# Optimization experiments

Measured on AMD Instinct MI355X. Metric: run time of the kernel, lower is better.

The kernel has to match this reference:

```python
import jax, jax.numpy as jnp
import numpy as np

IDIM = 128
ODIM = 128
G = 8          # deformable groups
KH = KW = 3
K = KH * KW


def conv3x3(x, w, b):
    # x: [B,C,H,W], w: [O,I,3,3], stride 1, pad 1
    y = jax.lax.conv_general_dilated(x, w, (1, 1), ((1, 1), (1, 1)),
                                     dimension_numbers=('NCHW', 'OIHW', 'NCHW'))
    return y + b[None, :, None, None]


def deform_conv_v2(x, offset, mask, w, b):
    # x: [B,C,H,W]; offset: [B,2*G*K,H,W]; mask: [B,G*K,H,W] (pre-sigmoid)
    B, C, H, W = x.shape
    Cg = C // G
    off = offset.reshape(B, G, 2 * K, H, W)
    dy = off[:, :, 0::2]            # [B,G,K,H,W]
    dx = off[:, :, 1::2]
    m = jax.nn.sigmoid(mask).reshape(B, G, K, H, W)

    ky, kx = jnp.meshgrid(jnp.arange(KH), jnp.arange(KW), indexing='ij')
    ky = ky.reshape(K).astype(x.dtype)
    kx = kx.reshape(K).astype(x.dtype)
    hh = jnp.arange(H, dtype=x.dtype)
    ww = jnp.arange(W, dtype=x.dtype)
    # sampling positions (stride 1, pad 1, dilation 1)
    py = dy + (ky[:, None, None] + hh[None, :, None] - 1.0)   # [B,G,K,H,W]
    px = dx + (kx[:, None, None] + ww[None, None, :] - 1.0)

    y0 = jnp.floor(py)
    x0 = jnp.floor(px)
    ly = py - y0
    lx = px - x0

    x_flat = x.reshape(B, G, Cg, H * W)

    def gather(yi, xi):
        valid = ((yi >= 0) & (yi < H) & (xi >= 0) & (xi < W)).astype(x.dtype)
        yc = jnp.clip(yi, 0, H - 1).astype(jnp.int32)
        xc = jnp.clip(xi, 0, W - 1).astype(jnp.int32)
        idx = (yc * W + xc).reshape(B, G, 1, K * H * W)
        v = jnp.take_along_axis(x_flat, jnp.broadcast_to(idx, (B, G, Cg, K * H * W)), axis=3)
        return v.reshape(B, G, Cg, K, H, W) * valid[:, :, None]

    # bilinear interpolation with zero padding, fused with modulation mask
    v = (gather(y0, x0) * ((1 - ly) * (1 - lx))[:, :, None]
         + gather(y0, x0 + 1) * ((1 - ly) * lx)[:, :, None]
         + gather(y0 + 1, x0) * (ly * (1 - lx))[:, :, None]
         + gather(y0 + 1, x0 + 1) * (ly * lx)[:, :, None])
    v = v * m[:, :, None]                                      # [B,G,Cg,K,H,W]

    wr = w.reshape(w.shape[0], G, Cg, K)
    out = jnp.einsum('bgckhw,ogck->bohw', v, wr)
    return out + b[None, :, None, None]


def setup_inputs() -> dict:
    key = jax.random.key(0)
    ks = jax.random.split(key, 12)
    B, H, W = 2, 96, 96
    s = 0.05
    return {
        'R1': jax.random.normal(ks[0], (B, IDIM, H, W), jnp.float32),
        'Q0': jax.random.normal(ks[1], (B, IDIM, H, W), jnp.float32),
        'w1': jax.random.normal(ks[2], (ODIM, IDIM, 3, 3), jnp.float32) * s,
        'b1': jax.random.normal(ks[3], (ODIM,), jnp.float32) * s,
        'w2': jax.random.normal(ks[4], (ODIM, ODIM, 3, 3), jnp.float32) * s,
        'b2': jax.random.normal(ks[5], (ODIM,), jnp.float32) * s,
        'w_om': jax.random.normal(ks[6], (G * 3 * K, ODIM, 3, 3), jnp.float32) * s,
        'b_om': jax.random.normal(ks[7], (G * 3 * K,), jnp.float32) * s,
        'w_dcn': jax.random.normal(ks[8], (ODIM, IDIM, 3, 3), jnp.float32) * s,
        'b_dcn': jax.random.normal(ks[9], (ODIM,), jnp.float32) * s,
        'w_rq': jax.random.normal(ks[10], (ODIM, 2 * ODIM, 3, 3), jnp.float32) * s,
        'b_rq': jax.random.normal(ks[11], (ODIM,), jnp.float32) * s,
    }


def reference(R1, Q0, w1, b1, w2, b2, w_om, b_om, w_dcn, b_dcn, w_rq, b_rq):
    off = jax.nn.relu(conv3x3(R1 - Q0, w1, b1))
    off = jax.nn.relu(conv3x3(off, w2, b2))
    om = conv3x3(off, w_om, b_om)                 # [B, 3*G*K, H, W]
    o1, o2, mask = jnp.split(om, 3, axis=1)
    offset = jnp.concatenate([o1, o2], axis=1)    # [B, 2*G*K, H, W]
    fea = jax.nn.relu(deform_conv_v2(R1, offset, mask, w_dcn, b_dcn))
    fused = jnp.concatenate([fea, Q0], axis=1)
    return jax.nn.relu(conv3x3(fused, w_rq, b_rq))
```

## Files before the change

kernel.cpp:

```cpp
#include <hip/hip_runtime.h>

#define HH 96
#define WW 96
#define HW 9216
#define NPIX 18432
#define OMC 216
#define PP 9604

typedef __attribute__((ext_vector_type(8))) short short8x;
typedef __attribute__((ext_vector_type(8))) unsigned short ushort8x;
typedef __attribute__((ext_vector_type(4))) float f32x4;

__device__ __forceinline__ f32x4 mfma16(short8x a, short8x b, f32x4 c) {
    return __builtin_amdgcn_mfma_f32_16x16x32_bf16(a, b, c, 0, 0, 0);
}
__device__ __forceinline__ unsigned short f2bf(float f) {
    unsigned int u = __float_as_uint(f);
    u = (u + 0x7FFFu + ((u >> 16) & 1u)) >> 16;
    return (unsigned short)u;
}
__device__ __forceinline__ float bf2f(unsigned short b) {
    return __uint_as_float((unsigned int)b << 16);
}
__device__ __forceinline__ void split2(float v, unsigned short& h, unsigned short& l) {
    h = f2bf(v);
    l = f2bf(v - bf2f(h));
}
__device__ __forceinline__ void gld_lds16(const unsigned short* src, unsigned short* dst) {
    __builtin_amdgcn_global_load_lds(
        (const __attribute__((address_space(1))) unsigned int*)src,
        (__attribute__((address_space(3))) unsigned int*)dst, 16, 0, 0);
}

__global__ __launch_bounds__(256) void zero_borders(
    unsigned short* __restrict__ diffb,
    unsigned short* __restrict__ t1,
    unsigned short* __restrict__ catb)
{
    int i = blockIdx.x * 256 + threadIdx.x;
    if (i >= 776) return;
    int b = i / 388, r = i % 388;
    int y, x;
    if      (r < 98)  { y = 0;          x = r; }
    else if (r < 196) { y = 97;         x = r - 98; }
    else if (r < 292) { y = r - 196 + 1; x = 0; }
    else              { y = r - 292 + 1; x = 97; }
    size_t P = (size_t)b * PP + (size_t)y * 98 + x;
    ushort8x z = {};
    #pragma unroll
    for (int c = 0; c < 32; ++c) *(ushort8x*)&diffb[P * 256 + c * 8] = z;
    #pragma unroll
    for (int c = 0; c < 32; ++c) *(ushort8x*)&t1[P * 256 + c * 8] = z;
    #pragma unroll
    for (int c = 0; c < 64; ++c) *(ushort8x*)&catb[P * 512 + c * 8] = z;
}

__global__ __launch_bounds__(256) void prep_acts(
    const float* __restrict__ R1, const float* __restrict__ Q0,
    unsigned short* __restrict__ r1b,
    unsigned short* __restrict__ diffb,
    unsigned short* __restrict__ cat)
{
    __shared__ float tR[128][64];
    __shared__ float tQ[128][64];
    int tid = threadIdx.x;
    int p0  = blockIdx.x * 64;
    int b   = p0 / HW;
    int rem0 = p0 % HW;

    for (int e = tid; e < 2048; e += 256) {
        int c = e >> 4, j = e & 15;
        size_t base = ((size_t)(b * 128 + c)) * HW + rem0;
        *(float4*)&tR[c][j * 4] = *(const float4*)(R1 + base + j * 4);
        *(float4*)&tQ[c][j * 4] = *(const float4*)(Q0 + base + j * 4);
    }
    __syncthreads();

    int p = tid & 63, half = tid >> 6;
    int c0 = half * 32;
    int pix = p0 + p;
    int rm = pix % HW, yy = rm / 96, xx = rm % 96;
    size_t P = (size_t)b * PP + (size_t)(yy + 1) * 98 + xx + 1;
    ushort8x rb[4], dh[4], dl[4], qh[4], ql[4];
    #pragma unroll
    for (int cc = 0; cc < 32; ++cc) {
        float r = tR[c0 + cc][p], q = tQ[c0 + cc][p];
        rb[cc >> 3][cc & 7] = f2bf(r);
        unsigned short h, l;
        split2(r - q, h, l); dh[cc >> 3][cc & 7] = h; dl[cc >> 3][cc & 7] = l;
        split2(q, h, l);     qh[cc >> 3][cc & 7] = h; ql[cc >> 3][cc & 7] = l;
    }
    #pragma unroll
    for (int i = 0; i < 4; ++i) {
        *(ushort8x*)&r1b[(size_t)pix * 128 + c0 + i * 8] = rb[i];
        *(ushort8x*)&diffb[P * 256 +       c0 + i * 8] = dh[i];
        *(ushort8x*)&diffb[P * 256 + 128 + c0 + i * 8] = dl[i];
        *(ushort8x*)&cat [P * 512 + 128 + c0 + i * 8] = qh[i];
        *(ushort8x*)&cat [P * 512 + 384 + c0 + i * 8] = ql[i];
    }
}

__global__ __launch_bounds__(256) void prep_w(
    const float* __restrict__ w1, const float* __restrict__ w2,
    const float* __restrict__ wom, const float* __restrict__ bom,
    const float* __restrict__ wrq, const float* __restrict__ wdcn,
    unsigned short* __restrict__ p1, unsigned short* __restrict__ p2,
    unsigned short* __restrict__ pom, unsigned short* __restrict__ prq,
    unsigned short* __restrict__ pdcn, float* __restrict__ bomp)
{
    int idx = blockIdx.x * 256 + threadIdx.x;
    unsigned short h, l;
    if (idx < 147456) {
        int t = idx / 16384, o = (idx >> 7) & 127, ci = idx & 127;
        int src = (o * 128 + ci) * 9 + t;
        split2(w1[src], h, l);  p1[idx] = h;  p1[idx + 147456] = l;
        split2(w2[src], h, l);  p2[idx] = h;  p2[idx + 147456] = l;
        int dd = o * 1152 + ((ci >> 4) * 9 + t) * 16 + (ci & 15);
        split2(wdcn[src], h, l); pdcn[dd] = h; pdcn[dd + 147456] = l;
    }
    if (idx < 294912) {
        {
            int t = idx / 32768, o = (idx >> 7) & 255, ci = idx & 127;
            float v = (o < OMC) ? wom[(o * 128 + ci) * 9 + t] : 0.f;
            split2(v, h, l); pom[idx] = h; pom[idx + 294912] = l;
        }
        {
            int t = idx / 32768, o = (idx >> 8) & 127, ci = idx & 255;
            split2(wrq[(o * 256 + ci) * 9 + t], h, l);
            prq[idx] = h; prq[idx + 294912] = l;
        }
    }
    if (idx < 256) bomp[idx] = (idx < OMC) ? bom[idx] : 0.f;
}

template<int CIN, int COUTP, int MODE, bool RELU>
__global__ __launch_bounds__(256, 2) void conv_mfma(
    const unsigned short* __restrict__ in,
    const unsigned short* __restrict__ wpk,
    const float* __restrict__ bias,
    void* __restrict__ outv)
{
    constexpr int NKC = CIN / 32;
    constexpr int NSTEP = 9 * NKC;
    const size_t WPLANE = (size_t)9 * COUTP * CIN;

    __shared__ __align__(16) unsigned short s_buf[3][3072 + 8192];

    int tid = threadIdx.x;
    int wid = tid >> 6, lane = tid & 63;
    int r = lane & 15, q = lane >> 4;
    int bid = blockIdx.x;
    int swz = (bid & 7) * 48 + (bid >> 3);
    int rowid = swz >> 1, half = swz & 1;
    int b = rowid / 96, y = rowid % 96;
    int x0 = half * 48;
    int nbase = blockIdx.y * 128;

    auto stage = [&](int buf, int step) {
        int t = step / NKC, kc = step - t * NKC;
        int dy = t / 3 - 1, dx = t % 3 - 1;
        unsigned short* sb = &s_buf[buf][0];
        {
            int j = tid;
            int m = j >> 7, pl = (j >> 6) & 1, L = j & 63;
            int px = m * 16 + (L & 15), qd = L >> 4;
            const unsigned short* src = in +
                ((size_t)b * PP + (size_t)(y + 1 + dy) * 98 + (x0 + 1 + dx + px)) * (2 * CIN)
                + pl * CIN + kc * 32 + qd * 8;
            gld_lds16(src, sb + (size_t)(wid * 64) * 8);
        }
        if (tid < 128) {
            int j = 256 + tid;
            int m = j >> 7, pl = (j >> 6) & 1, L = j & 63;
            int px = m * 16 + (L & 15), qd = L >> 4;
            const unsigned short* src = in +
                ((size_t)b * PP + (size_t)(y + 1 + dy) * 98 + (x0 + 1 + dx + px)) * (2 * CIN)
                + pl * CIN + kc * 32 + qd * 8;
            gld_lds16(src, sb + (size_t)(256 + wid * 64) * 8);
        }
        const unsigned short* wbase = wpk + ((size_t)t * COUTP + nbase) * CIN + kc * 32;
        #pragma unroll
        for (int c = 0; c < 4; ++c) {
            int j = c * 256 + tid;
            int ni = (j >> 7) & 1, pl = (j >> 6) & 1, L = j & 63;
            int rr = L & 15, qq = L >> 4;
            const unsigned short* src = wbase + (size_t)pl * WPLANE
                + (size_t)(c * 32 + ni * 16 + rr) * CIN + qq * 8;
            gld_lds16(src, sb + 3072 + (size_t)(c * 256 + wid * 64) * 8);
        }
    };

    f32x4 acc[3][2] = {};

    auto compute = [&](int buf) {
        const unsigned short* sb = &s_buf[buf][0];
        short8x AH[3], AL[3], BH[2], BL[2];
        #pragma unroll
        for (int m = 0; m < 3; ++m) {
            AH[m] = *(const short8x*)(sb + m * 1024 + lane * 8);
            AL[m] = *(const short8x*)(sb + m * 1024 + 512 + lane * 8);
        }
        #pragma unroll
        for (int n = 0; n < 2; ++n) {
            BH[n] = *(const short8x*)(sb + 3072 + wid * 2048 + n * 1024 + lane * 8);
            BL[n] = *(const short8x*)(sb + 3072 + wid * 2048 + n * 1024 + 512 + lane * 8);
        }
        #pragma unroll
        for (int m = 0; m < 3; ++m) {
            #pragma unroll
            for (int n = 0; n < 2; ++n) {
                acc[m][n] = mfma16(AH[m], BH[n], acc[m][n]);
                acc[m][n] = mfma16(AL[m], BH[n], acc[m][n]);
                acc[m][n] = mfma16(AH[m], BL[n], acc[m][n]);
            }
        }
    };

    stage(0, 0);
    stage(1, 1);
    if (tid < 128) asm volatile("s_waitcnt vmcnt(6)" ::: "memory");
    else           asm volatile("s_waitcnt vmcnt(5)" ::: "memory");
    __builtin_amdgcn_s_barrier();

    for (int k = 0; k < NSTEP; ++k) {
        const int nb = k + 2;
        if (nb < NSTEP) stage(nb % 3, nb);
        compute(k % 3);
        if (k + 1 < NSTEP) {
            if (nb < NSTEP) {
                if (tid < 128) asm volatile("s_waitcnt vmcnt(6)" ::: "memory");
                else           asm volatile("s_waitcnt vmcnt(5)" ::: "memory");
            } else {
                asm volatile("s_waitcnt vmcnt(0)" ::: "memory");
            }
            __builtin_amdgcn_s_barrier();
        }
    }

    #pragma unroll
    for (int m = 0; m < 3; ++m) {
        #pragma unroll
        for (int n = 0; n < 2; ++n) {
            int o = nbase + wid * 32 + n * 16 + r;
            float bv = bias[o];
            #pragma unroll
            for (int j = 0; j < 4; ++j) {
                int px = m * 16 + q * 4 + j;
                int xx = x0 + px;
                float v = acc[m][n][j] + bv;
                if (RELU) v = fmaxf(v, 0.f);
                if (MODE == 0) {
                    size_t P = (size_t)b * PP + (size_t)(y + 1) * 98 + xx + 1;
                    unsigned short h, l; split2(v, h, l);
                    ((unsigned short*)outv)[P * 2 * COUTP + o] = h;
                    ((unsigned short*)outv)[P * 2 * COUTP + COUTP + o] = l;
                } else if (MODE == 1) {
                    if (o < OMC)
                        ((unsigned short*)outv)[((size_t)b * HW + y * 96 + xx) * OMC + o] = f2bf(v);
                } else {
                    ((float*)outv)[((size_t)b * 128 + o) * HW + y * 96 + xx] = v;
                }
            }
        }
    }
}

__global__ __launch_bounds__(256, 3) void deform_mfma(
    const unsigned short* __restrict__ xb,
    const unsigned short* __restrict__ omf,
    const unsigned short* __restrict__ wpk,
    const float* __restrict__ bias,
    unsigned short* __restrict__ cat)
{
    __shared__ __align__(16) unsigned short s_v[16][1160];
    __shared__ __align__(16) unsigned short s_om[16][216];

    int tid = threadIdx.x;
    int bid = blockIdx.x;
    int swzb = (bid & 7) * 144 + (bid >> 3);
    int pix0 = swzb * 16;
    int b = pix0 / HW;

    for (int it = tid; it < 432; it += 256) {
        int p = it / 27, j = it - p * 27;
        *(ushort8x*)&s_om[p][j * 8] =
            *(const ushort8x*)&omf[(size_t)(pix0 + p) * OMC + j * 8];
    }
    __syncthreads();

    for (int e = tid; e < 1152; e += 256) {
        int p = e & 15, gk = e >> 4;
        int pix = pix0 + p;
        int rem = pix % HW;
        int hh = rem / 96, ww = rem % 96;
        int g = gk / 9, k = gk % 9;
        const unsigned short* op = &s_om[p][0];
        float dy = bf2f(op[g * 18 + 2 * k]);
        float dx = bf2f(op[g * 18 + 2 * k + 1]);
        float mr = bf2f(op[144 + g * 9 + k]);
        float m = 1.f / (1.f + __expf(-mr));
        float py = dy + (float)(k / 3) + (float)hh - 1.f;
        float px = dx + (float)(k % 3) + (float)ww - 1.f;
        float fy = floorf(py), fx = floorf(px);
        int y0 = (int)fy, x0 = (int)fx;
        float ly = py - fy, lx = px - fx;
        float cw[4] = {(1.f - ly) * (1.f - lx), (1.f - ly) * lx,
                       ly * (1.f - lx), ly * lx};
        ushort8x cv0[4], cv1[4];
        #pragma unroll
        for (int j = 0; j < 4; ++j) {
            int yy = y0 + (j >> 1), xx = x0 + (j & 1);
            bool valid = ((unsigned)yy < 96u) && ((unsigned)xx < 96u);
            int yc = min(max(yy, 0), 95), xc = min(max(xx, 0), 95);
            const unsigned short* cp =
                xb + ((size_t)(b * HW + yc * 96 + xc)) * 128 + g * 16;
            cv0[j] = *(const ushort8x*)cp;
            cv1[j] = *(const ushort8x*)(cp + 8);
            cw[j] = valid ? cw[j] * m : 0.f;
        }
        ushort8x o0, o1;
        #pragma unroll
        for (int i = 0; i < 8; ++i) {
            float v0 = cw[0] * bf2f(cv0[0][i]) + cw[1] * bf2f(cv0[1][i])
                     + cw[2] * bf2f(cv0[2][i]) + cw[3] * bf2f(cv0[3][i]);
            float v1 = cw[0] * bf2f(cv1[0][i]) + cw[1] * bf2f(cv1[1][i])
                     + cw[2] * bf2f(cv1[2][i]) + cw[3] * bf2f(cv1[3][i]);
            o0[i] = f2bf(v0);
            o1[i] = f2bf(v1);
        }
        *(ushort8x*)&s_v[p][gk * 16    ] = o0;
        *(ushort8x*)&s_v[p][gk * 16 + 8] = o1;
    }
    __syncthreads();

    int wid = tid >> 6, lane = tid & 63;
    int r = lane & 15, q = lane >> 4;
    int n0 = wid * 32;
    f32x4 acc0 = {}, acc1 = {};
    const unsigned short* wb = wpk + (size_t)(n0 + r) * 1152 + q * 8;
    #pragma unroll
    for (int kp = 0; kp < 18; ++kp) {
        const int k0 = kp * 2, k1 = k0 + 1;
        short8x a0 = *(const short8x*)&s_v[r][k0 * 32 + q * 8];
        short8x a1 = *(const short8x*)&s_v[r][k1 * 32 + q * 8];
        short8x w00 = *(const short8x*)(wb + k0 * 32);
        short8x w10 = *(const short8x*)(wb + (size_t)16 * 1152 + k0 * 32);
        short8x l00 = *(const short8x*)(wb + 147456 + k0 * 32);
        short8x l10 = *(const short8x*)(wb + 147456 + (size_t)16 * 1152 + k0 * 32);
        short8x w01 = *(const short8x*)(wb + k1 * 32);
        short8x w11 = *(const short8x*)(wb + (size_t)16 * 1152 + k1 * 32);
        short8x l01 = *(const short8x*)(wb + 147456 + k1 * 32);
        short8x l11 = *(const short8x*)(wb + 147456 + (size_t)16 * 1152 + k1 * 32);
        acc0 = mfma16(a0, w00, acc0);
        acc1 = mfma16(a0, w10, acc1);
        acc0 = mfma16(a0, l00, acc0);
        acc1 = mfma16(a0, l10, acc1);
        acc0 = mfma16(a1, w01, acc0);
        acc1 = mfma16(a1, w11, acc1);
        acc0 = mfma16(a1, l01, acc0);
        acc1 = mfma16(a1, l11, acc1);
    }
    #pragma unroll
    for (int ni = 0; ni < 2; ++ni) {
        f32x4 A = ni ? acc1 : acc0;
        int o = n0 + ni * 16 + r;
        float bv = bias[o];
        #pragma unroll
        for (int j = 0; j < 4; ++j) {
            int pixel = pix0 + q * 4 + j;
            int bb = pixel / HW, rm = pixel % HW;
            int yy = rm / 96, xx = rm % 96;
            size_t P = (size_t)bb * PP + (size_t)(yy + 1) * 98 + xx + 1;
            float v = fmaxf(A[j] + bv, 0.f);
            unsigned short h, l;
            split2(v, h, l);
            cat[P * 512 + o] = h;
            cat[P * 512 + 256 + o] = l;
        }
    }
}

extern "C" void kernel_launch(void* const* d_in, const int* in_sizes, int n_in,
                              void* d_out, int out_size, void* d_ws, size_t ws_size,
                              hipStream_t stream) {
    const float* R1    = (const float*)d_in[0];
    const float* Q0    = (const float*)d_in[1];
    const float* w1    = (const float*)d_in[2];
    const float* b1    = (const float*)d_in[3];
    const float* w2    = (const float*)d_in[4];
    const float* b2    = (const float*)d_in[5];
    const float* w_om  = (const float*)d_in[6];
    const float* b_om  = (const float*)d_in[7];
    const float* w_dcn = (const float*)d_in[8];
    const float* b_dcn = (const float*)d_in[9];
    const float* w_rq  = (const float*)d_in[10];
    const float* b_rq  = (const float*)d_in[11];
    float* outp = (float*)d_out;

    char* w = (char*)d_ws;
    unsigned short* r1b   = (unsigned short*)w; w += (size_t)NPIX * 128 * 2;
    unsigned short* diffb = (unsigned short*)w; w += (size_t)2 * PP * 256 * 2;
    unsigned short* t1    = (unsigned short*)w; w += (size_t)2 * PP * 256 * 2;
    unsigned short* catb  = (unsigned short*)w; w += (size_t)2 * PP * 512 * 2;
    unsigned short* p1    = (unsigned short*)w; w += 2 * 147456 * 2;
    unsigned short* p2    = (unsigned short*)w; w += 2 * 147456 * 2;
    unsigned short* pdcn  = (unsigned short*)w; w += 2 * 147456 * 2;
    unsigned short* pom   = (unsigned short*)w; w += 2 * 294912 * 2;
    unsigned short* prq   = (unsigned short*)w; w += 2 * 294912 * 2;
    float*          bomp  = (float*)w;          w += 256 * 4;
    unsigned short* t2    = diffb;
    unsigned short* omf   = t1;

    zero_borders<<<4, 256, 0, stream>>>(diffb, t1, catb);
    prep_acts<<<288, 256, 0, stream>>>(R1, Q0, r1b, diffb, catb);
    prep_w<<<1152, 256, 0, stream>>>(w1, w2, w_om, b_om, w_rq, w_dcn,
                                     p1, p2, pom, prq, pdcn, bomp);

    conv_mfma<128, 128, 0, true ><<<dim3(384, 1), 256, 0, stream>>>(diffb, p1, b1, t1);
    conv_mfma<128, 128, 0, true ><<<dim3(384, 1), 256, 0, stream>>>(t1,    p2, b2, t2);
    conv_mfma<128, 256, 1, false><<<dim3(384, 2), 256, 0, stream>>>(t2,   pom, bomp, omf);

    deform_mfma<<<1152, 256, 0, stream>>>(r1b, omf, pdcn, b_dcn, catb);

    conv_mfma<256, 128, 2, true ><<<dim3(384, 1), 256, 0, stream>>>(catb, prq, b_rq, outp);
}
```

Baseline: 403.7 us.

## Double deform block pixel tile and split K into two halves

The deform kernel now processes 32 pixels per 512-thread block instead of 16 per 256-thread block. Eight waves are arranged as 2 pixel groups by 4 output groups, so each weight fragment fetched from global memory is shared by twice as many pixels. The sampled-value tile is built and consumed in two K halves, which keeps shared memory near its previous size but adds an extra barrier. The aim is to cut redundant weight loads, at the cost of fewer blocks and more synchronisation per block.

```diff
diff --git a/kernel.cpp b/kernel.cpp
--- a/kernel.cpp
+++ b/kernel.cpp
@@ -265,101 +265,110 @@
     }
 }
 
-__global__ __launch_bounds__(256, 3) void deform_mfma(
+__global__ __launch_bounds__(512, 4) void deform_mfma(
     const unsigned short* __restrict__ xb,
     const unsigned short* __restrict__ omf,
     const unsigned short* __restrict__ wpk,
     const float* __restrict__ bias,
     unsigned short* __restrict__ cat)
 {
-    __shared__ __align__(16) unsigned short s_v[16][1160];
-    __shared__ __align__(16) unsigned short s_om[16][216];
+    __shared__ __align__(16) unsigned short s_v[32][584];
+    __shared__ __align__(16) unsigned short s_om[32][220];
 
     int tid = threadIdx.x;
     int bid = blockIdx.x;
-    int swzb = (bid & 7) * 144 + (bid >> 3);
-    int pix0 = swzb * 16;
+    int swzb = (bid & 7) * 72 + (bid >> 3);
+    int pix0 = swzb * 32;
     int b = pix0 / HW;
 
-    for (int it = tid; it < 432; it += 256) {
+    for (int it = tid; it < 864; it += 512) {
         int p = it / 27, j = it - p * 27;
         *(ushort8x*)&s_om[p][j * 8] =
             *(const ushort8x*)&omf[(size_t)(pix0 + p) * OMC + j * 8];
     }
     __syncthreads();
 
-    for (int e = tid; e < 1152; e += 256) {
-        int p = e & 15, gk = e >> 4;
-        int pix = pix0 + p;
-        int rem = pix % HW;
-        int hh = rem / 96, ww = rem % 96;
-        int g = gk / 9, k = gk % 9;
-        const unsigned short* op = &s_om[p][0];
-        float dy = bf2f(op[g * 18 + 2 * k]);
-        float dx = bf2f(op[g * 18 + 2 * k + 1]);
-        float mr = bf2f(op[144 + g * 9 + k]);
-        float m = 1.f / (1.f + __expf(-mr));
-        float py = dy + (float)(k / 3) + (float)hh - 1.f;
-        float px = dx + (float)(k % 3) + (float)ww - 1.f;
-        float fy = floorf(py), fx = floorf(px);
-        int y0 = (int)fy, x0 = (int)fx;
-        float ly = py - fy, lx = px - fx;
-        float cw[4] = {(1.f - ly) * (1.f - lx), (1.f - ly) * lx,
-                       ly * (1.f - lx), ly * lx};
-        ushort8x cv0[4], cv1[4];
-        #pragma unroll
-        for (int j = 0; j < 4; ++j) {
-            int yy = y0 + (j >> 1), xx = x0 + (j & 1);
-            bool valid = ((unsigned)yy < 96u) && ((unsigned)xx < 96u);
-            int yc = min(max(yy, 0), 95), xc = min(max(xx, 0), 95);
-            const unsigned short* cp =
-                xb + ((size_t)(b * HW + yc * 96 + xc)) * 128 + g * 16;
-            cv0[j] = *(const ushort8x*)cp;
-            cv1[j] = *(const ushort8x*)(cp + 8);
-            cw[j] = valid ? cw[j] * m : 0.f;
-        }
-        ushort8x o0, o1;
-        #pragma unroll
-        for (int i = 0; i < 8; ++i) {
-            float v0 = cw[0] * bf2f(cv0[0][i]) + cw[1] * bf2f(cv0[1][i])
-                     + cw[2] * bf2f(cv0[2][i]) + cw[3] * bf2f(cv0[3][i]);
-            float v1 = cw[0] * bf2f(cv1[0][i]) + cw[1] * bf2f(cv1[1][i])
-                     + cw[2] * bf2f(cv1[2][i]) + cw[3] * bf2f(cv1[3][i]);
-            o0[i] = f2bf(v0);
-            o1[i] = f2bf(v1);
-        }
-        *(ushort8x*)&s_v[p][gk * 16    ] = o0;
-        *(ushort8x*)&s_v[p][gk * 16 + 8] = o1;
-    }
-    __syncthreads();
-
     int wid = tid >> 6, lane = tid & 63;
     int r = lane & 15, q = lane >> 4;
-    int n0 = wid * 32;
+    int mg = wid >> 2, ng = wid & 3;
+    int n0 = ng * 32;
     f32x4 acc0 = {}, acc1 = {};
     const unsigned short* wb = wpk + (size_t)(n0 + r) * 1152 + q * 8;
-    #pragma unroll
-    for (int kp = 0; kp < 18; ++kp) {
-        const int k0 = kp * 2, k1 = k0 + 1;
-        short8x a0 = *(const short8x*)&s_v[r][k0 * 32 + q * 8];
-        short8x a1 = *(const short8x*)&s_v[r][k1 * 32 + q * 8];
-        short8x w00 = *(const short8x*)(wb + k0 * 32);
-        short8x w10 = *(const short8x*)(wb + (size_t)16 * 1152 + k0 * 32);
-        short8x l00 = *(const short8x*)(wb + 147456 + k0 * 32);
-        short8x l10 = *(const short8x*)(wb + 147456 + (size_t)16 * 1152 + k0 * 32);
-        short8x w01 = *(const short8x*)(wb + k1 * 32);
-        short8x w11 = *(const short8x*)(wb + (size_t)16 * 1152 + k1 * 32);
-        short8x l01 = *(const short8x*)(wb + 147456 + k1 * 32);
-        short8x l11 = *(const short8x*)(wb + 147456 + (size_t)16 * 1152 + k1 * 32);
-        acc0 = mfma16(a0, w00, acc0);
-        acc1 = mfma16(a0, w10, acc1);
-        acc0 = mfma16(a0, l00, acc0);
-        acc1 = mfma16(a0, l10, acc1);
-        acc0 = mfma16(a1, w01, acc0);
-        acc1 = mfma16(a1, w11, acc1);
-        acc0 = mfma16(a1, l01, acc0);
-        acc1 = mfma16(a1, l11, acc1);
-    }
+
+    #pragma unroll
+    for (int h = 0; h < 2; ++h) {
+        for (int e = tid; e < 1152; e += 512) {
+            int p = e & 31, gkl = e >> 5;
+            int gk = h * 36 + gkl;
+            int pix = pix0 + p;
+            int rem = pix % HW;
+            int hh = rem / 96, ww = rem % 96;
+            int g = gk / 9, k = gk % 9;
+            const unsigned short* op = &s_om[p][0];
+            float dy = bf2f(op[g * 18 + 2 * k]);
+            float dx = bf2f(op[g * 18 + 2 * k + 1]);
+            float mr = bf2f(op[144 + g * 9 + k]);
+            float m = 1.f / (1.f + __expf(-mr));
+            float py = dy + (float)(k / 3) + (float)hh - 1.f;
+            float px = dx + (float)(k % 3) + (float)ww - 1.f;
+            float fy = floorf(py), fx = floorf(px);
+            int y0 = (int)fy, x0 = (int)fx;
+            float ly = py - fy, lx = px - fx;
+            float cw[4] = {(1.f - ly) * (1.f - lx), (1.f - ly) * lx,
+                           ly * (1.f - lx), ly * lx};
+            ushort8x cv0[4], cv1[4];
+            #pragma unroll
+            for (int j = 0; j < 4; ++j) {
+                int yy = y0 + (j >> 1), xx = x0 + (j & 1);
+                bool valid = ((unsigned)yy < 96u) && ((unsigned)xx < 96u);
+                int yc = min(max(yy, 0), 95), xc = min(max(xx, 0), 95);
+                const unsigned short* cp =
+                    xb + ((size_t)(b * HW + yc * 96 + xc)) * 128 + g * 16;
+                cv0[j] = *(const ushort8x*)cp;
+                cv1[j] = *(const ushort8x*)(cp + 8);
+                cw[j] = valid ? cw[j] * m : 0.f;
+            }
+            ushort8x o0, o1;
+            #pragma unroll
+            for (int i = 0; i < 8; ++i) {
+                float v0 = cw[0] * bf2f(cv0[0][i]) + cw[1] * bf2f(cv0[1][i])
+                         + cw[2] * bf2f(cv0[2][i]) + cw[3] * bf2f(cv0[3][i]);
+                float v1 = cw[0] * bf2f(cv1[0][i]) + cw[1] * bf2f(cv1[1][i])
+                         + cw[2] * bf2f(cv1[2][i]) + cw[3] * bf2f(cv1[3][i]);
+                o0[i] = f2bf(v0);
+                o1[i] = f2bf(v1);
+            }
+            *(ushort8x*)&s_v[p][gkl * 16    ] = o0;
+            *(ushort8x*)&s_v[p][gkl * 16 + 8] = o1;
+        }
+        __syncthreads();
+
+        #pragma unroll
+        for (int kpl = 0; kpl < 9; ++kpl) {
+            const int k0 = h * 18 + kpl * 2, k1 = k0 + 1;
+            const int c0 = kpl * 64;
+            short8x a0 = *(const short8x*)&s_v[mg * 16 + r][c0 + q * 8];
+            short8x a1 = *(const short8x*)&s_v[mg * 16 + r][c0 + 32 + q * 8];
+            short8x w00 = *(const short8x*)(wb + k0 * 32);
+            short8x w10 = *(const short8x*)(wb + (size_t)16 * 1152 + k0 * 32);
+            short8x l00 = *(const short8x*)(wb + 147456 + k0 * 32);
+            short8x l10 = *(const short8x*)(wb + 147456 + (size_t)16 * 1152 + k0 * 32);
+            short8x w01 = *(const short8x*)(wb + k1 * 32);
+            short8x w11 = *(const short8x*)(wb + (size_t)16 * 1152 + k1 * 32);
+            short8x l01 = *(const short8x*)(wb + 147456 + k1 * 32);
+            short8x l11 = *(const short8x*)(wb + 147456 + (size_t)16 * 1152 + k1 * 32);
+            acc0 = mfma16(a0, w00, acc0);
+            acc1 = mfma16(a0, w10, acc1);
+            acc0 = mfma16(a0, l00, acc0);
+            acc1 = mfma16(a0, l10, acc1);
+            acc0 = mfma16(a1, w01, acc0);
+            acc1 = mfma16(a1, w11, acc1);
+            acc0 = mfma16(a1, l01, acc0);
+            acc1 = mfma16(a1, l11, acc1);
+        }
+        if (h == 0) __syncthreads();
+    }
+
     #pragma unroll
     for (int ni = 0; ni < 2; ++ni) {
         f32x4 A = ni ? acc1 : acc0;
@@ -367,15 +376,15 @@
         float bv = bias[o];
         #pragma unroll
         for (int j = 0; j < 4; ++j) {
-            int pixel = pix0 + q * 4 + j;
+            int pixel = pix0 + mg * 16 + q * 4 + j;
             int bb = pixel / HW, rm = pixel % HW;
             int yy = rm / 96, xx = rm % 96;
             size_t P = (size_t)bb * PP + (size_t)(yy + 1) * 98 + xx + 1;
             float v = fmaxf(A[j] + bv, 0.f);
-            unsigned short h, l;
-            split2(v, h, l);
-            cat[P * 512 + o] = h;
-            cat[P * 512 + 256 + o] = l;
+            unsigned short h2, l2;
+            split2(v, h2, l2);
+            cat[P * 512 + o] = h2;
+            cat[P * 512 + 256 + o] = l2;
         }
     }
 }
@@ -420,7 +429,7 @@
     conv_mfma<128, 128, 0, true ><<<dim3(384, 1), 256, 0, stream>>>(t1,    p2, b2, t2);
     conv_mfma<128, 256, 1, false><<<dim3(384, 2), 256, 0, stream>>>(t2,   pom, bomp, omf);
 
-    deform_mfma<<<1152, 256, 0, stream>>>(r1b, omf, pdcn, b_dcn, catb);
+    deform_mfma<<<576, 512, 0, stream>>>(r1b, omf, pdcn, b_dcn, catb);
 
     conv_mfma<256, 128, 2, true ><<<dim3(384, 1), 256, 0, stream>>>(catb, prq, b_rq, outp);
 }
```

Measured after the change: 422.1 us, median of 2. 4.6% more time.
